# Performance work log

Measured on AMD Instinct MI355X. Metric: run time of the kernel, lower is better.

The kernel has to match this reference:

```python
import jax, jax.numpy as jnp
import numpy as np

N, H, W = 2, 64, 64
HM, WM = 2 * H - 1, 2 * W - 1


def setup_inputs() -> dict:
    key = jax.random.key(0)
    x = jax.random.normal(key, (N, HM * WM, H, W), dtype=jnp.float32)
    return {"x": x}


def reference(x):
    n, c, h_feat, w_feat = x.shape
    hm, wm = 2 * h_feat - 1, 2 * w_feat - 1
    xr = x.reshape(n, hm, wm, h_feat, w_feat)
    xt = jnp.transpose(xr, (0, 3, 4, 1, 2))
    hh = jnp.arange(h_feat)
    ww = jnp.arange(w_feat)
    idxh = hh[None, :] - hh[:, None] + (h_feat - 1)
    idxw = ww[None, :] - ww[:, None] + (w_feat - 1)
    a = jnp.take_along_axis(xt, idxh[None, :, None, :, None], axis=3)
    out = jnp.take_along_axis(a, idxw[None, None, :, None, :], axis=4)
    return out.reshape(n, h_feat * w_feat, h_feat, w_feat)
```

## Files before the change

kernel.cpp:

```cpp
#include <hip/hip_runtime.h>


#define PSA_H 64
#define PSA_W 64
#define PSA_HM 127
#define PSA_WM 127
#define PSA_HW (PSA_H * PSA_W)
#define PSA_CHW (PSA_HM * PSA_WM)
#define NPAIR 4

__global__ __launch_bounds__(512) void psa_distribute_kernel(
    const float* __restrict__ in, float* __restrict__ out) {
    __shared__ float lds[NPAIR * PSA_HW];

    const int b   = blockIdx.x;
    const int xcd = b & 7;
    const int s   = (xcd << 8) + (b >> 3);
    const int n   = s >> 10;
    const int u   = (s >> 4) & 63;
    const int h0  = (s & 15) << 2;

    size_t in_base[NPAIR];
    size_t out_base[NPAIR];
#pragma unroll
    for (int p = 0; p < NPAIR; ++p) {
        const int h  = h0 + p;
        const int i  = (h + u) & 63;
        const int di = i - h + (PSA_H - 1);
        in_base[p]  = ((size_t)n * PSA_CHW + (size_t)di * PSA_WM) * PSA_HW
                      + (size_t)h * PSA_W;
        out_base[p] = ((size_t)n * PSA_HW + (size_t)h * PSA_W) * PSA_HW
                      + (size_t)i * PSA_W;
    }

    const int t     = threadIdx.x;
    const int wl    = t & 15;
    const int djo   = (t >> 4) & 3;
    const int wv    = t >> 6;
    const int wbase = wl << 2;

#pragma unroll
    for (int it = 0; it < 4; ++it) {
        const int dj = it * 32 + wv * 4 + djo;
        const bool row_ok = (dj < PSA_WM) &&
                            (wbase + 3 >= PSA_W - 1 - dj) &&
                            (wbase <= 2 * (PSA_W - 1) - dj);
        if (row_ok) {
            const int jb = dj + wbase - (PSA_W - 1);
#pragma unroll
            for (int p = 0; p < NPAIR; ++p) {
                const float4 v = *(const float4*)(
                    in + in_base[p] + (size_t)dj * PSA_HW + wbase);
#pragma unroll
                for (int e = 0; e < 4; ++e) {
                    const int j = jb + e;
                    if ((unsigned)j < (unsigned)PSA_W) {
                        lds[p * PSA_HW + (wbase + e) * PSA_W + j] =
                            ((const float*)&v)[e];
                    }
                }
            }
        }
    }
    __syncthreads();

    const float4* lds4 = (const float4*)lds;
#pragma unroll
    for (int it = 0; it < 8; ++it) {
        const int idx = it * 512 + t;
        const int p   = idx >> 10;
        const int rem = idx & 1023;
        const int w   = rem >> 4;
        const int j4  = rem & 15;
        float4* dst = (float4*)(out + out_base[p]);
        dst[w * (PSA_HW / 4) + j4] = lds4[idx];
    }
}

extern "C" void kernel_launch(void* const* d_in, const int* in_sizes, int n_in,
                              void* d_out, int out_size, void* d_ws, size_t ws_size,
                              hipStream_t stream) {
    const float* x = (const float*)d_in[0];
    float* out = (float*)d_out;
    const int nblocks = 2 * PSA_H * PSA_H / NPAIR;
    psa_distribute_kernel<<<nblocks, 512, 0, stream>>>(x, out);
}
```

Baseline: 81.95 us.

## Group four consecutive output rows per block for contiguous 1KB stores

Each block now handles a fixed h and four consecutive i values instead of four different h with skewed i. The four output rows for a given w then sit next to each other, so every store burst covers 1KB of contiguous memory instead of four scattered 256B rows. The block size also doubles to 1024 threads, halving the per-thread loop counts. The risk is lower occupancy with larger blocks, and different input access locality across blocks.

After: 73.81 us. 1.11x faster.

```diff
diff --git a/kernel.cpp b/kernel.cpp
--- a/kernel.cpp
+++ b/kernel.cpp
@@ -7,30 +7,26 @@
 #define PSA_WM 127
 #define PSA_HW (PSA_H * PSA_W)
 #define PSA_CHW (PSA_HM * PSA_WM)
-#define NPAIR 4
+#define NI 4
 
-__global__ __launch_bounds__(512) void psa_distribute_kernel(
+__global__ __launch_bounds__(1024) void psa_distribute_kernel(
     const float* __restrict__ in, float* __restrict__ out) {
-    __shared__ float lds[NPAIR * PSA_HW];
+    __shared__ float lds[NI * PSA_HW];
 
     const int b   = blockIdx.x;
     const int xcd = b & 7;
     const int s   = (xcd << 8) + (b >> 3);
     const int n   = s >> 10;
-    const int u   = (s >> 4) & 63;
-    const int h0  = (s & 15) << 2;
+    const int r   = s & 1023;
+    const int h   = r >> 4;
+    const int i0  = (r & 15) << 2;
 
-    size_t in_base[NPAIR];
-    size_t out_base[NPAIR];
+    size_t in_base[NI];
 #pragma unroll
-    for (int p = 0; p < NPAIR; ++p) {
-        const int h  = h0 + p;
-        const int i  = (h + u) & 63;
-        const int di = i - h + (PSA_H - 1);
-        in_base[p]  = ((size_t)n * PSA_CHW + (size_t)di * PSA_WM) * PSA_HW
-                      + (size_t)h * PSA_W;
-        out_base[p] = ((size_t)n * PSA_HW + (size_t)h * PSA_W) * PSA_HW
-                      + (size_t)i * PSA_W;
+    for (int p = 0; p < NI; ++p) {
+        const int di = i0 + p - h + (PSA_H - 1);
+        in_base[p] = ((size_t)n * PSA_CHW + (size_t)di * PSA_WM) * PSA_HW
+                     + (size_t)h * PSA_W;
     }
 
     const int t     = threadIdx.x;
@@ -40,15 +36,15 @@
     const int wbase = wl << 2;
 
 #pragma unroll
-    for (int it = 0; it < 4; ++it) {
-        const int dj = it * 32 + wv * 4 + djo;
+    for (int it = 0; it < 2; ++it) {
+        const int dj = it * 64 + wv * 4 + djo;
         const bool row_ok = (dj < PSA_WM) &&
                             (wbase + 3 >= PSA_W - 1 - dj) &&
                             (wbase <= 2 * (PSA_W - 1) - dj);
         if (row_ok) {
             const int jb = dj + wbase - (PSA_W - 1);
 #pragma unroll
-            for (int p = 0; p < NPAIR; ++p) {
+            for (int p = 0; p < NI; ++p) {
                 const float4 v = *(const float4*)(
                     in + in_base[p] + (size_t)dj * PSA_HW + wbase);
 #pragma unroll
@@ -64,16 +60,20 @@
     }
     __syncthreads();
 
+    const size_t out4_base0 =
+        ((size_t)n * PSA_HW + (size_t)h * PSA_W) * (PSA_HW / 4)
+        + (size_t)i0 * 16;
+
     const float4* lds4 = (const float4*)lds;
 #pragma unroll
-    for (int it = 0; it < 8; ++it) {
-        const int idx = it * 512 + t;
-        const int p   = idx >> 10;
-        const int rem = idx & 1023;
-        const int w   = rem >> 4;
-        const int j4  = rem & 15;
-        float4* dst = (float4*)(out + out_base[p]);
-        dst[w * (PSA_HW / 4) + j4] = lds4[idx];
+    for (int it = 0; it < 4; ++it) {
+        const int idx = it * 1024 + t;
+        const int w   = idx >> 6;
+        const int l   = idx & 63;
+        const int p   = l >> 4;
+        const int j4  = l & 15;
+        float4* dst = (float4*)out + out4_base0 + (size_t)w * (PSA_HW / 4);
+        dst[l] = lds4[p * (PSA_HW / 4) + w * 16 + j4];
     }
 }
 
@@ -82,6 +82,6 @@
                               hipStream_t stream) {
     const float* x = (const float*)d_in[0];
     float* out = (float*)d_out;
-    const int nblocks = 2 * PSA_H * PSA_H / NPAIR;
-    psa_distribute_kernel<<<nblocks, 512, 0, stream>>>(x, out);
+    const int nblocks = 2 * PSA_H * PSA_H / NI;
+    psa_distribute_kernel<<<nblocks, 1024, 0, stream>>>(x, out);
 }
```
